# Performance work log

Hardware: AMD Instinct MI355X
Metric: run time of the kernel (lower is better)

Reference implementation:

```python
import jax, jax.numpy as jnp
import numpy as np

B, S, H = 32, 512, 1024
N_CAND = 256
NUM_LABELS = 34


def setup_inputs() -> dict:
    key = jax.random.key(0)
    k1, k2, k3, k4 = jax.random.split(key, 4)
    hidden = jax.random.normal(k1, (B, S, H), dtype=jnp.float32)
    W = jax.random.normal(k2, (2 * H, NUM_LABELS), dtype=jnp.float32) * 0.02
    b = jnp.zeros((NUM_LABELS,), dtype=jnp.float32)
    cand_batch = jax.random.randint(k3, (N_CAND,), 0, B, dtype=jnp.int32)
    # cut positions in [1, S-1] so both left and right segments are non-empty
    cand_cut = jax.random.randint(k4, (N_CAND,), 1, S, dtype=jnp.int32)
    return {"hidden": hidden, "W": W, "b": b,
            "cand_batch": cand_batch, "cand_cut": cand_cut}


def reference(hidden, W, b, cand_batch, cand_cut):
    # hidden: [B, S, H]; cand_batch/cand_cut: [N]
    S_ = hidden.shape[1]
    x = hidden[cand_batch]                      # [N, S, H] per-candidate sequence
    pos = jnp.arange(S_)                        # [S]
    left = (pos[None, :, None] < cand_cut[:, None, None])  # [N, S, 1]
    neg = jnp.finfo(hidden.dtype).min
    pooledL = jnp.max(jnp.where(left, x, neg), axis=1)      # [N, H] max over tokens < cut
    pooledR = jnp.max(jnp.where(left, neg, x), axis=1)      # [N, H] max over tokens >= cut
    pooled = jnp.concatenate([pooledL, pooledR], axis=-1)   # [N, 2H]
    logits = pooled @ W + b                                  # [N, num_labels]
    return logits
```

## Files before the change

### kernel.cpp

```cpp
#include <hip/hip_runtime.h>
#include <cfloat>


constexpr int S_LEN  = 512;
constexpr int HDIM   = 1024;
constexpr int NLAB   = 34;
constexpr int CHUNK  = 16;
constexpr int NCHUNK = S_LEN / CHUNK;

__device__ __forceinline__ void fmax4(float4& a, const float4 v) {
    a.x = fmaxf(a.x, v.x); a.y = fmaxf(a.y, v.y);
    a.z = fmaxf(a.z, v.z); a.w = fmaxf(a.w, v.w);
}

__global__ __launch_bounds__(256) void chunkmax_kernel(
    const float* __restrict__ hidden, float* __restrict__ ws)
{
    const int blk = blockIdx.x;
    const int b   = blk / NCHUNK;
    const int c   = blk % NCHUNK;
    const int t   = threadIdx.x;

    const float* base = hidden + ((size_t)b * S_LEN + (size_t)c * CHUNK) * HDIM + 4 * t;
    float4 m = make_float4(-FLT_MAX, -FLT_MAX, -FLT_MAX, -FLT_MAX);
    #pragma unroll
    for (int s = 0; s < CHUNK; ++s)
        fmax4(m, *reinterpret_cast<const float4*>(base + (size_t)s * HDIM));

    *reinterpret_cast<float4*>(ws + ((size_t)b * NCHUNK + c) * HDIM + 4 * t) = m;
}

__global__ __launch_bounds__(256) void pool_gemm_kernel(
    const float* __restrict__ hidden,
    const float* __restrict__ ws,
    const float* __restrict__ W,
    const float* __restrict__ bias,
    const int*   __restrict__ cand_batch,
    const int*   __restrict__ cand_cut,
    float*       __restrict__ out)
{
    __shared__ float pooled[2 * HDIM];
    __shared__ float partial[4][NLAB];

    const int n   = blockIdx.x;
    const int t   = threadIdx.x;
    const int b   = cand_batch[n];
    const int cut = cand_cut[n];
    const int fcL = cut / CHUNK;
    const int fcR = (cut + CHUNK - 1) / CHUNK;

    const float* hbase  = hidden + (size_t)b * S_LEN * HDIM + 4 * t;
    const float* wsbase = ws + (size_t)b * NCHUNK * HDIM + 4 * t;

    float4 mL = make_float4(-FLT_MAX, -FLT_MAX, -FLT_MAX, -FLT_MAX);
    float4 mR = mL;

    #pragma unroll 4
    for (int c = 0; c < fcL; ++c)
        fmax4(mL, *reinterpret_cast<const float4*>(wsbase + (size_t)c * HDIM));
    #pragma unroll 4
    for (int s = fcL * CHUNK; s < cut; ++s)
        fmax4(mL, *reinterpret_cast<const float4*>(hbase + (size_t)s * HDIM));

    #pragma unroll 4
    for (int s = cut; s < fcR * CHUNK; ++s)
        fmax4(mR, *reinterpret_cast<const float4*>(hbase + (size_t)s * HDIM));
    #pragma unroll 4
    for (int c = fcR; c < NCHUNK; ++c)
        fmax4(mR, *reinterpret_cast<const float4*>(wsbase + (size_t)c * HDIM));

    *reinterpret_cast<float4*>(&pooled[4 * t])        = mL;
    *reinterpret_cast<float4*>(&pooled[HDIM + 4 * t]) = mR;
    __syncthreads();

    const int w    = t >> 6;
    const int lane = t & 63;
    if (lane < NLAB) {
        const int k0 = w * (2 * HDIM / 4);
        float acc = 0.0f;
        #pragma unroll 8
        for (int k = k0; k < k0 + (2 * HDIM / 4); ++k)
            acc = fmaf(pooled[k], W[(size_t)k * NLAB + lane], acc);
        partial[w][lane] = acc;
    }
    __syncthreads();

    if (t < NLAB) {
        out[(size_t)n * NLAB + t] =
            partial[0][t] + partial[1][t] + partial[2][t] + partial[3][t] + bias[t];
    }
}

__global__ __launch_bounds__(256) void dmbert_pool_gemm(
    const float* __restrict__ hidden,
    const float* __restrict__ W,
    const float* __restrict__ bias,
    const int*   __restrict__ cand_batch,
    const int*   __restrict__ cand_cut,
    float*       __restrict__ out)
{
    __shared__ float pooled[2 * HDIM];
    __shared__ float partial[4][NLAB];

    const int n   = blockIdx.x;
    const int t   = threadIdx.x;
    const int bi  = cand_batch[n];
    const int cut = cand_cut[n];

    const float* base = hidden + (size_t)bi * S_LEN * HDIM + 4 * t;
    float4 mL = make_float4(-FLT_MAX, -FLT_MAX, -FLT_MAX, -FLT_MAX);
    float4 mR = mL;

    #pragma unroll 4
    for (int s = 0; s < cut; ++s)
        fmax4(mL, *reinterpret_cast<const float4*>(base + (size_t)s * HDIM));
    #pragma unroll 4
    for (int s = cut; s < S_LEN; ++s)
        fmax4(mR, *reinterpret_cast<const float4*>(base + (size_t)s * HDIM));

    *reinterpret_cast<float4*>(&pooled[4 * t])        = mL;
    *reinterpret_cast<float4*>(&pooled[HDIM + 4 * t]) = mR;
    __syncthreads();

    const int w    = t >> 6;
    const int lane = t & 63;
    if (lane < NLAB) {
        const int k0 = w * (2 * HDIM / 4);
        float acc = 0.0f;
        #pragma unroll 8
        for (int k = k0; k < k0 + (2 * HDIM / 4); ++k)
            acc = fmaf(pooled[k], W[(size_t)k * NLAB + lane], acc);
        partial[w][lane] = acc;
    }
    __syncthreads();

    if (t < NLAB) {
        out[(size_t)n * NLAB + t] =
            partial[0][t] + partial[1][t] + partial[2][t] + partial[3][t] + bias[t];
    }
}

extern "C" void kernel_launch(void* const* d_in, const int* in_sizes, int n_in,
                              void* d_out, int out_size, void* d_ws, size_t ws_size,
                              hipStream_t stream) {
    const float* hidden = (const float*)d_in[0];
    const float* W      = (const float*)d_in[1];
    const float* bias   = (const float*)d_in[2];
    const int*   cb     = (const int*)d_in[3];
    const int*   cc     = (const int*)d_in[4];
    float*       outp   = (float*)d_out;

    const int ncand = in_sizes[3];
    const int B     = in_sizes[0] / (S_LEN * HDIM);
    const size_t ws_needed = (size_t)B * NCHUNK * HDIM * sizeof(float);

    if (ws_size >= ws_needed) {
        float* chunkmax = (float*)d_ws;
        chunkmax_kernel<<<B * NCHUNK, 256, 0, stream>>>(hidden, chunkmax);
        pool_gemm_kernel<<<ncand, 256, 0, stream>>>(hidden, chunkmax, W, bias, cb, cc, outp);
    } else {
        dmbert_pool_gemm<<<ncand, 256, 0, stream>>>(hidden, W, bias, cb, cc, outp);
    }
}
```

Measured before the change: 119.8 us.

## Split pooling and GEMV into separate kernels with finer column-parallel pooling

Pooling now runs on a 2D grid of candidates by four column quarters with 64-thread blocks, writing pooled vectors to workspace. A separate GEMV kernel then reads pooled rows as float4 and computes logits. The intent is more blocks in flight for the latency-bound gather over chunk maxima and raw rows. In exchange it adds a kernel launch and a global round trip for the pooled activations.

```diff
diff --git a/kernel.cpp b/kernel.cpp
--- a/kernel.cpp
+++ b/kernel.cpp
@@ -14,7 +14,7 @@
 }
 
 __global__ __launch_bounds__(256) void chunkmax_kernel(
-    const float* __restrict__ hidden, float* __restrict__ ws)
+    const float* __restrict__ hidden, float* __restrict__ ws0)
 {
     const int blk = blockIdx.x;
     const int b   = blk / NCHUNK;
@@ -27,37 +27,34 @@
     for (int s = 0; s < CHUNK; ++s)
         fmax4(m, *reinterpret_cast<const float4*>(base + (size_t)s * HDIM));
 
-    *reinterpret_cast<float4*>(ws + ((size_t)b * NCHUNK + c) * HDIM + 4 * t) = m;
+    *reinterpret_cast<float4*>(ws0 + ((size_t)b * NCHUNK + c) * HDIM + 4 * t) = m;
 }
 
-__global__ __launch_bounds__(256) void pool_gemm_kernel(
+__global__ __launch_bounds__(64) void pool_kernel(
     const float* __restrict__ hidden,
-    const float* __restrict__ ws,
-    const float* __restrict__ W,
-    const float* __restrict__ bias,
+    const float* __restrict__ ws0,
     const int*   __restrict__ cand_batch,
     const int*   __restrict__ cand_cut,
-    float*       __restrict__ out)
+    float*       __restrict__ pooled)
 {
-    __shared__ float pooled[2 * HDIM];
-    __shared__ float partial[4][NLAB];
-
     const int n   = blockIdx.x;
+    const int q   = blockIdx.y;
     const int t   = threadIdx.x;
+    const int col = q * 256 + 4 * t;
     const int b   = cand_batch[n];
     const int cut = cand_cut[n];
     const int fcL = cut / CHUNK;
     const int fcR = (cut + CHUNK - 1) / CHUNK;
 
-    const float* hbase  = hidden + (size_t)b * S_LEN * HDIM + 4 * t;
-    const float* wsbase = ws + (size_t)b * NCHUNK * HDIM + 4 * t;
+    const float* hbase = hidden + (size_t)b * S_LEN * HDIM + col;
+    const float* wbase = ws0 + (size_t)b * NCHUNK * HDIM + col;
 
     float4 mL = make_float4(-FLT_MAX, -FLT_MAX, -FLT_MAX, -FLT_MAX);
     float4 mR = mL;
 
     #pragma unroll 4
     for (int c = 0; c < fcL; ++c)
-        fmax4(mL, *reinterpret_cast<const float4*>(wsbase + (size_t)c * HDIM));
+        fmax4(mL, *reinterpret_cast<const float4*>(wbase + (size_t)c * HDIM));
     #pragma unroll 4
     for (int s = fcL * CHUNK; s < cut; ++s)
         fmax4(mL, *reinterpret_cast<const float4*>(hbase + (size_t)s * HDIM));
@@ -67,20 +64,40 @@
         fmax4(mR, *reinterpret_cast<const float4*>(hbase + (size_t)s * HDIM));
     #pragma unroll 4
     for (int c = fcR; c < NCHUNK; ++c)
-        fmax4(mR, *reinterpret_cast<const float4*>(wsbase + (size_t)c * HDIM));
+        fmax4(mR, *reinterpret_cast<const float4*>(wbase + (size_t)c * HDIM));
 
-    *reinterpret_cast<float4*>(&pooled[4 * t])        = mL;
-    *reinterpret_cast<float4*>(&pooled[HDIM + 4 * t]) = mR;
-    __syncthreads();
+    float* prow = pooled + (size_t)n * (2 * HDIM);
+    *reinterpret_cast<float4*>(prow + col)        = mL;
+    *reinterpret_cast<float4*>(prow + HDIM + col) = mR;
+}
 
+__global__ __launch_bounds__(256) void gemm_kernel(
+    const float* __restrict__ pooled,
+    const float* __restrict__ W,
+    const float* __restrict__ bias,
+    float*       __restrict__ out)
+{
+    __shared__ float partial[4][NLAB];
+
+    const int n    = blockIdx.x;
+    const int t    = threadIdx.x;
     const int w    = t >> 6;
     const int lane = t & 63;
+
     if (lane < NLAB) {
-        const int k0 = w * (2 * HDIM / 4);
+        const int k0 = w * 512;
+        const float4* p4 = reinterpret_cast<const float4*>(
+            pooled + (size_t)n * (2 * HDIM) + k0);
         float acc = 0.0f;
-        #pragma unroll 8
-        for (int k = k0; k < k0 + (2 * HDIM / 4); ++k)
-            acc = fmaf(pooled[k], W[(size_t)k * NLAB + lane], acc);
+        #pragma unroll 4
+        for (int kk = 0; kk < 128; ++kk) {
+            const float4 pv = p4[kk];
+            const int k = k0 + 4 * kk;
+            acc = fmaf(pv.x, W[(size_t)(k + 0) * NLAB + lane], acc);
+            acc = fmaf(pv.y, W[(size_t)(k + 1) * NLAB + lane], acc);
+            acc = fmaf(pv.z, W[(size_t)(k + 2) * NLAB + lane], acc);
+            acc = fmaf(pv.w, W[(size_t)(k + 3) * NLAB + lane], acc);
+        }
         partial[w][lane] = acc;
     }
     __syncthreads();
@@ -152,12 +169,15 @@
 
     const int ncand = in_sizes[3];
     const int B     = in_sizes[0] / (S_LEN * HDIM);
-    const size_t ws_needed = (size_t)B * NCHUNK * HDIM * sizeof(float);
+    const size_t cm_elems = (size_t)B * NCHUNK * HDIM;
+    const size_t ws_needed = (cm_elems + (size_t)ncand * 2 * HDIM) * sizeof(float);
 
     if (ws_size >= ws_needed) {
-        float* chunkmax = (float*)d_ws;
-        chunkmax_kernel<<<B * NCHUNK, 256, 0, stream>>>(hidden, chunkmax);
-        pool_gemm_kernel<<<ncand, 256, 0, stream>>>(hidden, chunkmax, W, bias, cb, cc, outp);
+        float* cm     = (float*)d_ws;
+        float* pooled = cm + cm_elems;
+        chunkmax_kernel<<<B * NCHUNK, 256, 0, stream>>>(hidden, cm);
+        pool_kernel<<<dim3(ncand, 4), 64, 0, stream>>>(hidden, cm, cb, cc, pooled);
+        gemm_kernel<<<ncand, 256, 0, stream>>>(pooled, W, bias, outp);
     } else {
         dmbert_pool_gemm<<<ncand, 256, 0, stream>>>(hidden, W, bias, cb, cc, outp);
     }
```

Measured after the change: 116.7 us. 1.03x faster.

## Split per-candidate pooling across four thread groups with 1024-thread blocks

Applied to the files above, without the earlier changes.

The pooling kernel now launches 1024 threads per candidate. Four groups of 256 threads each stride over chunks and tokens and produce partial left/right maxima, which are reduced through shared memory. The GEMV is split across 16 waves of 128 rows each instead of 4 waves of 512. The aim is to expose more memory-level parallelism and shorten the serial dependency chain per candidate, since only 256 blocks cover the GPU. The cost is more shared memory, extra barriers and reduction steps.

```diff
diff --git a/kernel.cpp b/kernel.cpp
--- a/kernel.cpp
+++ b/kernel.cpp
@@ -14,7 +14,7 @@
 }
 
 __global__ __launch_bounds__(256) void chunkmax_kernel(
-    const float* __restrict__ hidden, float* __restrict__ ws)
+    const float* __restrict__ hidden, float* __restrict__ ws0)
 {
     const int blk = blockIdx.x;
     const int b   = blk / NCHUNK;
@@ -27,67 +27,85 @@
     for (int s = 0; s < CHUNK; ++s)
         fmax4(m, *reinterpret_cast<const float4*>(base + (size_t)s * HDIM));
 
-    *reinterpret_cast<float4*>(ws + ((size_t)b * NCHUNK + c) * HDIM + 4 * t) = m;
+    *reinterpret_cast<float4*>(ws0 + ((size_t)b * NCHUNK + c) * HDIM + 4 * t) = m;
 }
 
-__global__ __launch_bounds__(256) void pool_gemm_kernel(
+__global__ __launch_bounds__(1024) void pool_gemm2(
     const float* __restrict__ hidden,
-    const float* __restrict__ ws,
+    const float* __restrict__ ws0,
     const float* __restrict__ W,
     const float* __restrict__ bias,
     const int*   __restrict__ cand_batch,
     const int*   __restrict__ cand_cut,
     float*       __restrict__ out)
 {
+    __shared__ float partL[4][HDIM];
+    __shared__ float partR[4][HDIM];
     __shared__ float pooled[2 * HDIM];
-    __shared__ float partial[4][NLAB];
+    __shared__ float gpart[16][NLAB];
 
     const int n   = blockIdx.x;
     const int t   = threadIdx.x;
+    const int g   = t >> 8;
+    const int tt  = t & 255;
+    const int col = 4 * tt;
     const int b   = cand_batch[n];
     const int cut = cand_cut[n];
-    const int fcL = cut / CHUNK;
-    const int fcR = (cut + CHUNK - 1) / CHUNK;
+    const int fcL = cut >> 4;
+    const int fcR = (cut + CHUNK - 1) >> 4;
 
-    const float* hbase  = hidden + (size_t)b * S_LEN * HDIM + 4 * t;
-    const float* wsbase = ws + (size_t)b * NCHUNK * HDIM + 4 * t;
+    const float* hbase = hidden + (size_t)b * S_LEN * HDIM + col;
+    const float* wbase = ws0 + (size_t)b * NCHUNK * HDIM + col;
 
     float4 mL = make_float4(-FLT_MAX, -FLT_MAX, -FLT_MAX, -FLT_MAX);
     float4 mR = mL;
 
-    #pragma unroll 4
-    for (int c = 0; c < fcL; ++c)
-        fmax4(mL, *reinterpret_cast<const float4*>(wsbase + (size_t)c * HDIM));
-    #pragma unroll 4
-    for (int s = fcL * CHUNK; s < cut; ++s)
+    #pragma unroll 2
+    for (int c = g; c < fcL; c += 4)
+        fmax4(mL, *reinterpret_cast<const float4*>(wbase + (size_t)c * HDIM));
+    const int c0 = fcR + ((g - fcR) & 3);
+    #pragma unroll 2
+    for (int c = c0; c < NCHUNK; c += 4)
+        fmax4(mR, *reinterpret_cast<const float4*>(wbase + (size_t)c * HDIM));
+
+    #pragma unroll 2
+    for (int s = fcL * CHUNK + g; s < cut; s += 4)
         fmax4(mL, *reinterpret_cast<const float4*>(hbase + (size_t)s * HDIM));
+    #pragma unroll 2
+    for (int s = cut + g; s < fcR * CHUNK; s += 4)
+        fmax4(mR, *reinterpret_cast<const float4*>(hbase + (size_t)s * HDIM));
 
-    #pragma unroll 4
-    for (int s = cut; s < fcR * CHUNK; ++s)
-        fmax4(mR, *reinterpret_cast<const float4*>(hbase + (size_t)s * HDIM));
-    #pragma unroll 4
-    for (int c = fcR; c < NCHUNK; ++c)
-        fmax4(mR, *reinterpret_cast<const float4*>(wsbase + (size_t)c * HDIM));
+    *reinterpret_cast<float4*>(&partL[g][col]) = mL;
+    *reinterpret_cast<float4*>(&partR[g][col]) = mR;
+    __syncthreads();
 
-    *reinterpret_cast<float4*>(&pooled[4 * t])        = mL;
-    *reinterpret_cast<float4*>(&pooled[HDIM + 4 * t]) = mR;
+    {
+        const int j = t;
+        pooled[j] = fmaxf(fmaxf(partL[0][j], partL[1][j]),
+                          fmaxf(partL[2][j], partL[3][j]));
+        pooled[HDIM + j] = fmaxf(fmaxf(partR[0][j], partR[1][j]),
+                                 fmaxf(partR[2][j], partR[3][j]));
+    }
     __syncthreads();
 
     const int w    = t >> 6;
     const int lane = t & 63;
     if (lane < NLAB) {
-        const int k0 = w * (2 * HDIM / 4);
+        const float* p = pooled + 128 * w;
+        const float* Wp = W + (size_t)(128 * w) * NLAB + lane;
         float acc = 0.0f;
         #pragma unroll 8
-        for (int k = k0; k < k0 + (2 * HDIM / 4); ++k)
-            acc = fmaf(pooled[k], W[(size_t)k * NLAB + lane], acc);
-        partial[w][lane] = acc;
+        for (int k = 0; k < 128; ++k)
+            acc = fmaf(p[k], Wp[(size_t)k * NLAB], acc);
+        gpart[w][lane] = acc;
     }
     __syncthreads();
 
     if (t < NLAB) {
-        out[(size_t)n * NLAB + t] =
-            partial[0][t] + partial[1][t] + partial[2][t] + partial[3][t] + bias[t];
+        float s = bias[t];
+        #pragma unroll
+        for (int w2 = 0; w2 < 16; ++w2) s += gpart[w2][t];
+        out[(size_t)n * NLAB + t] = s;
     }
 }
 
@@ -155,9 +173,9 @@
     const size_t ws_needed = (size_t)B * NCHUNK * HDIM * sizeof(float);
 
     if (ws_size >= ws_needed) {
-        float* chunkmax = (float*)d_ws;
-        chunkmax_kernel<<<B * NCHUNK, 256, 0, stream>>>(hidden, chunkmax);
-        pool_gemm_kernel<<<ncand, 256, 0, stream>>>(hidden, chunkmax, W, bias, cb, cc, outp);
+        float* cm = (float*)d_ws;
+        chunkmax_kernel<<<B * NCHUNK, 256, 0, stream>>>(hidden, cm);
+        pool_gemm2<<<ncand, 1024, 0, stream>>>(hidden, cm, W, bias, cb, cc, outp);
     } else {
         dmbert_pool_gemm<<<ncand, 256, 0, stream>>>(hidden, W, bias, cb, cc, outp);
     }
```

New measurement: 107.5 us. 1.11x faster.
